# Optimization experiments

Hardware: AMD Instinct MI355X
Metric: run time of the kernel (lower is better)

The kernel has to match this reference:

```python
import jax, jax.numpy as jnp
import numpy as np


def bilinear_resize(x, out_h, out_w):
    # x: [B, C, H, W]; matches torch F.interpolate(mode='bilinear', align_corners=False)
    B, C, H, W = x.shape
    ry = jnp.clip((jnp.arange(out_h, dtype=jnp.float32) + 0.5) * (H / out_h) - 0.5, 0.0, H - 1)
    rx = jnp.clip((jnp.arange(out_w, dtype=jnp.float32) + 0.5) * (W / out_w) - 0.5, 0.0, W - 1)
    y0 = jnp.floor(ry).astype(jnp.int32); y1 = jnp.minimum(y0 + 1, H - 1)
    x0 = jnp.floor(rx).astype(jnp.int32); x1 = jnp.minimum(x0 + 1, W - 1)
    wy = (ry - y0)[:, None]  # [out_h,1]
    wx = (rx - x0)[None, :]  # [1,out_w]
    r0 = x[:, :, y0, :]; r1 = x[:, :, y1, :]
    v00 = r0[:, :, :, x0]; v01 = r0[:, :, :, x1]
    v10 = r1[:, :, :, x0]; v11 = r1[:, :, :, x1]
    return (v00 * (1 - wx) + v01 * wx) * (1 - wy) + (v10 * (1 - wx) + v11 * wx) * wy


def setup_inputs() -> dict:
    key0 = jax.random.key(0)
    ks = jax.random.split(key0, 16)
    B, N, C, H = 2, 300, 256, 8
    hw_lvl = np.array([[64, 64], [32, 32], [16, 16]], dtype=np.int64)
    L = int((hw_lvl[:, 0] * hw_lvl[:, 1]).sum())  # 5376
    p = lambda k, sh: (0.02 * jax.random.normal(k, sh, dtype=jnp.float32))
    return {
        'query': jax.random.normal(ks[0], (B, N, C), dtype=jnp.float32),
        'key': jax.random.normal(ks[1], (B, L, C), dtype=jnp.float32),
        'value': jax.random.normal(ks[2], (B, L, C), dtype=jnp.float32),
        'key_padding_mask': jnp.zeros((B, L), dtype=bool),
        'hw_lvl': hw_lvl,
        'Wq': p(ks[3], (C, C)), 'Wk': p(ks[4], (C, C)), 'Wv': p(ks[5], (C, C)),
        'Wp': p(ks[6], (C, C)), 'bp': jnp.zeros((C,), jnp.float32),
        'W1': p(ks[7], (H, H)), 'b1': jnp.zeros((H,), jnp.float32),
        'W2': p(ks[8], (H, H)), 'b2': jnp.zeros((H,), jnp.float32),
        'W3': p(ks[9], (H, H)), 'b3': jnp.zeros((H,), jnp.float32),
        'Wm': p(ks[10], (3 * H, 1)), 'bm': jnp.zeros((1,), jnp.float32),
    }


def reference(query, key, value, key_padding_mask, hw_lvl,
              Wq, Wk, Wv, Wp, bp, W1, b1, W2, b2, W3, b3, Wm, bm):
    hw = np.asarray(hw_lvl)
    h1, wd1 = int(hw[0, 0]), int(hw[0, 1])
    h2, wd2 = int(hw[1, 0]), int(hw[1, 1])
    h3, wd3 = int(hw[2, 0]), int(hw[2, 1])
    w1 = h1 * wd1
    w2 = w1 + h2 * wd2
    B, N, C = query.shape
    L = key.shape[1]
    H = W1.shape[0]
    scale = (C // H) ** -0.5

    q = (query @ Wq).reshape(B, N, H, C // H)
    k = (key @ Wk).reshape(B, L, H, C // H)
    v = (value @ Wv).reshape(B, L, H, C // H)
    attn = jnp.einsum('bnhd,blhd->bhnl', q, k) * scale  # [B,H,N,L]

    ap = attn.transpose(0, 2, 3, 1)  # [B,N,L,H]
    f1 = jax.nn.relu(ap[:, :, :w1] @ W1 + b1)                      # [B,N,w1,H]
    f2 = jax.nn.relu(ap[:, :, w1:w2] @ W2 + b2)                    # [B,N,h2*wd2,H]
    f3 = jax.nn.relu(ap[:, :, w2:] @ W3 + b3)                      # [B,N,h3*wd3,H]
    f2 = f2.transpose(0, 1, 3, 2).reshape(B * N, H, h2, wd2)
    f3 = f3.transpose(0, 1, 3, 2).reshape(B * N, H, h3, wd3)
    f2 = bilinear_resize(f2, h1, wd1).transpose(0, 2, 3, 1).reshape(B, N, w1, H)
    f3 = bilinear_resize(f3, h1, wd1).transpose(0, 2, 3, 1).reshape(B, N, w1, H)
    new_feats = jnp.concatenate([f1, f2, f3], axis=-1)             # [B,N,w1,3H]
    mask = jax.nn.relu(new_feats @ Wm + bm)                        # [B,N,w1,1]

    aw = jax.nn.softmax(attn, axis=-1)                             # [B,H,N,L]
    x = jnp.einsum('bhnl,blhd->bnhd', aw, v).reshape(B, N, C)
    x = x @ Wp + bp
    return x, mask
```

## Files before the change

kernel.cpp:

```cpp
#include <hip/hip_runtime.h>
#include <hip/hip_bf16.h>

typedef __hip_bfloat16 bf16;
typedef __attribute__((ext_vector_type(8))) short short8v;
typedef __attribute__((ext_vector_type(8))) unsigned short ushort8v;
typedef __attribute__((ext_vector_type(4))) unsigned short ushort4v;
typedef __attribute__((ext_vector_type(4))) float float4v;

__device__ __forceinline__ float bfu2f(unsigned short u) {
    union { unsigned int i; float f; } v; v.i = ((unsigned int)u) << 16; return v.f;
}
__device__ __forceinline__ unsigned short f2bfu_rn(float x) {
    union { float f; unsigned int i; } u; u.f = x;
    unsigned int r = (u.i + 0x7FFFu + ((u.i >> 16) & 1u)) >> 16;
    return (unsigned short)r;
}

__global__ __launch_bounds__(256) void cast_wt(
    const float* __restrict__ Wq, const float* __restrict__ Wk,
    const float* __restrict__ Wv, const float* __restrict__ Wp,
    unsigned short* __restrict__ wt)
{
    __shared__ unsigned short tile[64][72];
    const float* W = (blockIdx.z == 0) ? Wq : (blockIdx.z == 1) ? Wk
                   : (blockIdx.z == 2) ? Wv : Wp;
    unsigned short* WT = wt + (size_t)blockIdx.z * 65536;
    const int t = threadIdx.x;
    const int k0 = blockIdx.x * 64, n0 = blockIdx.y * 64;
    {
        const int r = t >> 2, cseg = (t & 3) * 16;
        const float* src = W + (size_t)(k0 + r) * 256 + n0 + cseg;
        #pragma unroll
        for (int j = 0; j < 16; ++j) tile[r][cseg + j] = f2bfu_rn(src[j]);
    }
    __syncthreads();
    {
        const int ch = t & 63, lq = t >> 6;
        ushort8v o0, o1;
        #pragma unroll
        for (int i = 0; i < 8; ++i) o0[i] = tile[lq * 16 + i][ch];
        #pragma unroll
        for (int i = 0; i < 8; ++i) o1[i] = tile[lq * 16 + 8 + i][ch];
        unsigned short* dst = WT + (size_t)(n0 + ch) * 256 + k0 + lq * 16;
        *(ushort8v*)(dst)     = o0;
        *(ushort8v*)(dst + 8) = o1;
    }
}

__device__ __forceinline__ void proj_core(
    const float* __restrict__ aptr, const unsigned short* __restrict__ Wt,
    int nc0, int m16, int quad, float4v acc[8])
{
    #pragma unroll
    for (int i = 0; i < 8; ++i) acc[i] = (float4v){0.f, 0.f, 0.f, 0.f};
    #pragma unroll
    for (int ks = 0; ks < 8; ++ks) {
        float4 a0 = *(const float4*)(aptr + ks * 32);
        float4 a1 = *(const float4*)(aptr + ks * 32 + 4);
        short8v af;
        af[0] = (short)f2bfu_rn(a0.x); af[1] = (short)f2bfu_rn(a0.y);
        af[2] = (short)f2bfu_rn(a0.z); af[3] = (short)f2bfu_rn(a0.w);
        af[4] = (short)f2bfu_rn(a1.x); af[5] = (short)f2bfu_rn(a1.y);
        af[6] = (short)f2bfu_rn(a1.z); af[7] = (short)f2bfu_rn(a1.w);
        #pragma unroll
        for (int i = 0; i < 8; ++i) {
            short8v bfr = *(const short8v*)(Wt + (size_t)(nc0 + i * 16 + m16) * 256 + ks * 32 + quad * 8);
            acc[i] = __builtin_amdgcn_mfma_f32_16x16x32_bf16(af, bfr, acc[i], 0, 0, 0);
        }
    }
}

__global__ __launch_bounds__(256) void proj_all(
    const float* __restrict__ q, const float* __restrict__ k, const float* __restrict__ v,
    const unsigned short* __restrict__ wt,
    unsigned short* __restrict__ qb, unsigned short* __restrict__ kb,
    unsigned short* __restrict__ vt)
{
    const int t = threadIdx.x;
    const int wave = t >> 6, lane = t & 63;
    const int m16 = lane & 15, quad = lane >> 4;
    const int msub = (wave & 1) * 16;
    const int nc0 = (wave >> 1) * 128;
    const int bx = blockIdx.x;

    float4v acc[8];
    if (bx < 19) {
        const int m0 = bx * 32;
        const int arow = min(m0 + msub + m16, 599);
        proj_core(q + (size_t)arow * 256 + quad * 8, wt, nc0, m16, quad, acc);
        #pragma unroll
        for (int i = 0; i < 8; ++i)
            #pragma unroll
            for (int r = 0; r < 4; ++r) {
                int m = m0 + msub + quad * 4 + r;
                if (m < 600)
                    qb[(size_t)m * 256 + nc0 + i * 16 + m16] = f2bfu_rn(acc[i][r]);
            }
    } else if (bx < 355) {
        const int m0 = (bx - 19) * 32;
        proj_core(k + (size_t)(m0 + msub + m16) * 256 + quad * 8, wt + 65536, nc0, m16, quad, acc);
        const int bb = (m0 >= 5376) ? 1 : 0;
        const int lb0 = m0 - bb * 5376 + msub + quad * 4;
        const int hbase = (wave >> 1) * 4;
        #pragma unroll
        for (int i = 0; i < 8; ++i) {
            const int hh = hbase + (i >> 1);
            const int c16 = (i & 1) * 16;
            unsigned short* kdst = kb + ((size_t)(bb * 8 + hh) * 5376 + lb0) * 32 + c16 + m16;
            #pragma unroll
            for (int r = 0; r < 4; ++r)
                kdst[(size_t)r * 32] = f2bfu_rn(acc[i][r]);
        }
    } else {
        const int m0 = (bx - 355) * 32;
        proj_core(v + (size_t)(m0 + msub + m16) * 256 + quad * 8, wt + 131072, nc0, m16, quad, acc);
        const int bb = (m0 >= 5376) ? 1 : 0;
        const int lb0 = m0 - bb * 5376 + msub + quad * 4;
        const int g0 = lb0 >> 3, e0 = lb0 & 7;
        const int hbase = (wave >> 1) * 4;
        #pragma unroll
        for (int i = 0; i < 8; ++i) {
            const int hh = hbase + (i >> 1);
            const int cc = (i & 1) * 16 + m16;
            ushort4v p;
            #pragma unroll
            for (int r = 0; r < 4; ++r) p[r] = f2bfu_rn(acc[i][r]);
            *(ushort4v*)(vt + (((size_t)(bb * 8 + hh) * 672 + g0) * 32 + cc) * 8 + e0) = p;
        }
    }
}

__global__ __launch_bounds__(512) void attn_fused(
    const unsigned short* __restrict__ qb, const unsigned short* __restrict__ kb,
    const unsigned short* __restrict__ vt,
    const float* __restrict__ W1, const float* __restrict__ b1,
    const float* __restrict__ W2, const float* __restrict__ b2,
    const float* __restrict__ W3, const float* __restrict__ b3,
    const float* __restrict__ Wm,
    float* __restrict__ xbp, float* __restrict__ Sp,
    float* __restrict__ g2, float* __restrict__ g3, float* __restrict__ maskp)
{
    __shared__ unsigned short probs[8][16 * 136];
    __shared__ float wT[64];
    __shared__ float blv[8], wmv[8];

    const int t = threadIdx.x;
    const int wave = t >> 6, lane = t & 63;

    const int i0 = blockIdx.x;
    const int m = (i0 & 7) * 200 + (i0 >> 3);
    if (m >= 1596) return;
    const int grp = m / 19, nt = m - grp * 19;
    const int b = grp / 42, zz = grp - b * 42;
    const int n0 = nt * 16;
    const int l0 = zz * 128;
    const int lvl = (zz >= 32) + (zz >= 40);

    const float* Wl = (lvl == 0) ? W1 : (lvl == 1) ? W2 : W3;
    const float* bl = (lvl == 0) ? b1 : (lvl == 1) ? b2 : b3;
    if (t < 64) wT[t] = Wl[(t & 7) * 8 + (t >> 3)];
    if (t < 8)  { blv[t] = bl[t]; wmv[t] = Wm[lvl * 8 + t]; }

    const int m16 = lane & 15, quad = lane >> 4;
    const int h = wave;
    const float scale = 0.17677669529663687f;

    const unsigned short* kbase = kb + ((size_t)(b * 8 + h) * 5376 + l0) * 32 + quad * 8;
    const unsigned short* vtb = vt + ((size_t)(b * 8 + h) * 672 + (l0 >> 3)) * 256 + quad * 256 + m16 * 8;
    unsigned short* const pw = &probs[wave][0];

    short8v vb[8];
    #pragma unroll
    for (int s = 0; s < 4; ++s) {
        vb[2 * s]     = *(const short8v*)(vtb + s * 1024);
        vb[2 * s + 1] = *(const short8v*)(vtb + s * 1024 + 128);
    }
    const short8v qfrag = *(const short8v*)(qb + (size_t)(b * 300 + min(n0 + m16, 299)) * 256 + h * 32 + quad * 8);

    #pragma unroll
    for (int i = 0; i < 8; ++i) {
        short8v kf = *(const short8v*)(kbase + (size_t)(i * 16 + m16) * 32);
        float4v c = {0.f, 0.f, 0.f, 0.f};
        c = __builtin_amdgcn_mfma_f32_16x16x32_bf16(kf, qfrag, c, 0, 0, 0);
        ushort4v pk;
        #pragma unroll
        for (int r = 0; r < 4; ++r) pk[r] = f2bfu_rn(c[r] * scale);
        *(ushort4v*)(pw + m16 * 136 + i * 16 + quad * 4) = pk;
    }

    float4v c0 = {0.f, 0.f, 0.f, 0.f};
    float4v c1 = {0.f, 0.f, 0.f, 0.f};
    float sm0 = 0.f, sm1 = 0.f;
    #pragma unroll
    for (int step = 0; step < 4; ++step) {
        const int lloc = step * 32 + quad * 8;
        ushort8v ua = *(const ushort8v*)(pw + m16 * 136 + lloc);
        short8v af;
        #pragma unroll
        for (int j = 0; j < 8; ++j) {
            float e = __expf(bfu2f(ua[j]));
            if (j & 1) sm1 += e; else sm0 += e;
            af[j] = (short)f2bfu_rn(e);
        }
        c0 = __builtin_amdgcn_mfma_f32_16x16x32_bf16(af, vb[2 * step],     c0, 0, 0, 0);
        c1 = __builtin_amdgcn_mfma_f32_16x16x32_bf16(af, vb[2 * step + 1], c1, 0, 0, 0);
    }

    __syncthreads();

    {
        const int nl = t >> 5;
        const int n = n0 + nl;
        if (n < 300) {
            const int lb = (t & 31) * 4;
            ushort4v u[8];
            #pragma unroll
            for (int hp = 0; hp < 8; ++hp)
                u[hp] = *(const ushort4v*)(&probs[hp][nl * 136 + lb]);
            float4 o;
            float* op = (float*)&o;
            #pragma unroll
            for (int half = 0; half < 2; ++half) {
                float sv[2][8];
                #pragma unroll
                for (int pp = 0; pp < 2; ++pp)
                    #pragma unroll
                    for (int hp = 0; hp < 8; ++hp) sv[pp][hp] = bfu2f(u[hp][half * 2 + pp]);
                float f0 = 0.f, f1 = 0.f;
                #pragma unroll
                for (int hh = 0; hh < 8; ++hh) {
                    const float4 wA = *(const float4*)(&wT[hh * 8]);
                    const float4 wB = *(const float4*)(&wT[hh * 8 + 4]);
                    const float bb_ = blv[hh], wm_ = wmv[hh];
                    float a0 = bb_
                        + sv[0][0] * wA.x + sv[0][1] * wA.y + sv[0][2] * wA.z + sv[0][3] * wA.w
                        + sv[0][4] * wB.x + sv[0][5] * wB.y + sv[0][6] * wB.z + sv[0][7] * wB.w;
                    float a1 = bb_
                        + sv[1][0] * wA.x + sv[1][1] * wA.y + sv[1][2] * wA.z + sv[1][3] * wA.w
                        + sv[1][4] * wB.x + sv[1][5] * wB.y + sv[1][6] * wB.z + sv[1][7] * wB.w;
                    f0 += fmaxf(a0, 0.f) * wm_;
                    f1 += fmaxf(a1, 0.f) * wm_;
                }
                op[half * 2]     = f0;
                op[half * 2 + 1] = f1;
            }
            const size_t bn = (size_t)(b * 300 + n);
            const int p = l0 + lb;
            float* dst = (lvl == 0) ? maskp + bn * 4096 + p
                       : (lvl == 1) ? g2 + bn * 1024 + (p - 4096)
                       :              g3 + bn * 256  + (p - 5120);
            *(float4*)dst = o;
        }
    }

    float sm = sm0 + sm1;
    sm += __shfl_xor(sm, 16);
    sm += __shfl_xor(sm, 32);
    float* xplane = xbp + (size_t)zz * 153600;
    float* splane = Sp + (size_t)zz * 4800;
    if (lane < 16 && n0 + lane < 300)
        splane[(size_t)(b * 300 + n0 + lane) * 8 + h] = sm;
    #pragma unroll
    for (int r = 0; r < 4; ++r) {
        const int n = n0 + quad * 4 + r;
        if (n < 300) {
            float* o = xplane + (size_t)(b * 300 + n) * 256 + h * 32 + m16;
            o[0]  = c0[r];
            o[16] = c1[r];
        }
    }
}

__global__ __launch_bounds__(256) void finish(
    const float* __restrict__ g2, const float* __restrict__ g3,
    const float* __restrict__ xbp, const float* __restrict__ Sp,
    float* __restrict__ xr, float* __restrict__ Sr,
    const float* __restrict__ bmp, float* __restrict__ out)
{
    const int t = threadIdx.x;
    if (blockIdx.x < 600) {
        __shared__ float gs[1280];
        __shared__ float bms;
        const int bn = blockIdx.x;
        if (t == 0) bms = bmp[0];
        ((float4v*)gs)[t] = ((const float4v*)(g2 + (size_t)bn * 1024))[t];
        if (t < 64) ((float4v*)(gs + 1024))[t] = ((const float4v*)(g3 + (size_t)bn * 256))[t];
        __syncthreads();

        float* mp = out + 153600 + (size_t)bn * 4096;
        #pragma unroll
        for (int it = 0; it < 4; ++it) {
            const int p0 = it * 1024 + t * 4;
            float4v mv = *(const float4v*)(mp + p0);
            float4v res;
            #pragma unroll
            for (int pp = 0; pp < 4; ++pp) {
                const int p = p0 + pp;
                const int Y = p >> 6, X = p & 63;
                float acc = mv[pp] + bms;
                {
                    float ry = fminf(fmaxf(0.5f * Y - 0.25f, 0.f), 31.f);
                    float rx = fminf(fmaxf(0.5f * X - 0.25f, 0.f), 31.f);
                    int y0 = (int)ry, x0 = (int)rx;
                    int y1 = min(y0 + 1, 31), x1 = min(x0 + 1, 31);
                    float wy = ry - (float)y0, wx = rx - (float)x0;
                    acc += (gs[y0 * 32 + x0] * (1.f - wx) + gs[y0 * 32 + x1] * wx) * (1.f - wy)
                         + (gs[y1 * 32 + x0] * (1.f - wx) + gs[y1 * 32 + x1] * wx) * wy;
                }
                {
                    float ry = fminf(fmaxf(0.25f * Y - 0.375f, 0.f), 15.f);
                    float rx = fminf(fmaxf(0.25f * X - 0.375f, 0.f), 15.f);
                    int y0 = (int)ry, x0 = (int)rx;
                    int y1 = min(y0 + 1, 15), x1 = min(x0 + 1, 15);
                    float wy = ry - (float)y0, wx = rx - (float)x0;
                    acc += (gs[1024 + y0 * 16 + x0] * (1.f - wx) + gs[1024 + y0 * 16 + x1] * wx) * (1.f - wy)
                         + (gs[1024 + y1 * 16 + x0] * (1.f - wx) + gs[1024 + y1 * 16 + x1] * wx) * wy;
                }
                res[pp] = fmaxf(acc, 0.f);
            }
            *(float4v*)(mp + p0) = res;
        }
    } else {
        const int idx = (blockIdx.x - 600) * 256 + t;
        if (idx < 38400) {
            float4v s = {0.f, 0.f, 0.f, 0.f};
            #pragma unroll 7
            for (int z = 0; z < 42; ++z)
                s += *(const float4v*)(xbp + (size_t)z * 153600 + (size_t)idx * 4);
            *(float4v*)(xr + (size_t)idx * 4) = s;
        } else if (idx < 38400 + 1200) {
            const int si = (idx - 38400) * 4;
            float4v s = {0.f, 0.f, 0.f, 0.f};
            #pragma unroll 7
            for (int z = 0; z < 42; ++z)
                s += *(const float4v*)(Sp + (size_t)z * 4800 + si);
            *(float4v*)(Sr + si) = s;
        }
    }
}

__global__ __launch_bounds__(256) void proj_out(
    const float* __restrict__ xr, const float* __restrict__ Sr,
    const unsigned short* __restrict__ Wtp,
    const float* __restrict__ bpv, float* __restrict__ out)
{
    const int t = threadIdx.x;
    const int wave = t >> 6, lane = t & 63;
    const int m16 = lane & 15, quad = lane >> 4;
    const int nc0 = wave * 64;
    const int m0 = blockIdx.x * 16;
    const int arow = min(m0 + m16, 599);
    const float* a0p = xr + (size_t)arow * 256 + quad * 8;

    float4v acc[4];
    #pragma unroll
    for (int i = 0; i < 4; ++i) acc[i] = (float4v){0.f, 0.f, 0.f, 0.f};

    #pragma unroll
    for (int ks = 0; ks < 8; ++ks) {
        const float rS = 1.0f / Sr[(size_t)arow * 8 + ks];
        float4 x0 = *(const float4*)(a0p + ks * 32);
        float4 x1 = *(const float4*)(a0p + ks * 32 + 4);
        short8v af;
        af[0] = (short)f2bfu_rn(x0.x * rS); af[1] = (short)f2bfu_rn(x0.y * rS);
        af[2] = (short)f2bfu_rn(x0.z * rS); af[3] = (short)f2bfu_rn(x0.w * rS);
        af[4] = (short)f2bfu_rn(x1.x * rS); af[5] = (short)f2bfu_rn(x1.y * rS);
        af[6] = (short)f2bfu_rn(x1.z * rS); af[7] = (short)f2bfu_rn(x1.w * rS);
        #pragma unroll
        for (int i = 0; i < 4; ++i) {
            short8v bfr = *(const short8v*)(Wtp + (size_t)(nc0 + i * 16 + m16) * 256 + ks * 32 + quad * 8);
            acc[i] = __builtin_amdgcn_mfma_f32_16x16x32_bf16(af, bfr, acc[i], 0, 0, 0);
        }
    }

    #pragma unroll
    for (int i = 0; i < 4; ++i) {
        const float bv = bpv[nc0 + i * 16 + m16];
        #pragma unroll
        for (int r = 0; r < 4; ++r) {
            int mm = m0 + quad * 4 + r;
            if (mm < 600)
                out[(size_t)mm * 256 + nc0 + i * 16 + m16] = acc[i][r] + bv;
        }
    }
}

extern "C" void kernel_launch(void* const* d_in, const int* in_sizes, int n_in,
                              void* d_out, int out_size, void* d_ws, size_t ws_size,
                              hipStream_t stream) {
    const float* query = (const float*)d_in[0];
    const float* key   = (const float*)d_in[1];
    const float* value = (const float*)d_in[2];
    const float* Wq = (const float*)d_in[5];
    const float* Wk = (const float*)d_in[6];
    const float* Wv = (const float*)d_in[7];
    const float* Wp = (const float*)d_in[8];
    const float* bp = (const float*)d_in[9];
    const float* W1 = (const float*)d_in[10];
    const float* b1 = (const float*)d_in[11];
    const float* W2 = (const float*)d_in[12];
    const float* b2 = (const float*)d_in[13];
    const float* W3 = (const float*)d_in[14];
    const float* b3 = (const float*)d_in[15];
    const float* Wm = (const float*)d_in[16];
    const float* bm = (const float*)d_in[17];
    float* out = (float*)d_out;

    char* ws = (char*)d_ws;
    unsigned short* wt = (unsigned short*)(ws);
    bf16*  qb   = (bf16*) (ws + 524288);
    bf16*  kb   = (bf16*) (ws + 831488);
    bf16*  vt   = (bf16*) (ws + 6336512);
    float* xbp  = (float*)(ws + 11841536);
    float* Sp   = (float*)(ws + 37646336);
    float* g2   = (float*)(ws + 38452736);
    float* g3   = (float*)(ws + 40910336);
    float* xr   = (float*)(ws + 41524736);
    float* Sr   = (float*)(ws + 42139136);
    float* maskp = out + 153600;

    cast_wt<<<dim3(4, 4, 4), 256, 0, stream>>>(Wq, Wk, Wv, Wp, wt);

    proj_all<<<691, 256, 0, stream>>>(query, key, value, wt,
        (unsigned short*)qb, (unsigned short*)kb, (unsigned short*)vt);

    attn_fused<<<1600, 512, 0, stream>>>(
        (const unsigned short*)qb, (const unsigned short*)kb, (const unsigned short*)vt,
        W1, b1, W2, b2, W3, b3, Wm, xbp, Sp, g2, g3, maskp);

    finish<<<755, 256, 0, stream>>>(g2, g3, xbp, Sp, xr, Sr, bm, out);

    proj_out<<<38, 256, 0, stream>>>(xr, Sr, (const unsigned short*)wt + 196608, bp, out);
}
```

Before: 189.1 us.

## Fuse split-K reduction with output projection and store partials before mask stage

The separate proj_out kernel is merged into finish: each of 38 extra blocks reduces the 42 split-K partial planes for its 16 rows straight into shared memory, then runs the bf16 MFMA projection in the same block. This removes one kernel launch and the xr/Sr round trip through global memory. The per-head partial x and softmax-sum stores in attn_fused now happen before the barrier and mask epilogue, so they can overlap with the mask work. In exchange, the reduction now runs on only 38 blocks instead of about 155, which may lower memory parallelism for the roughly 26MB partial read.

```diff
diff --git a/kernel.cpp b/kernel.cpp
--- a/kernel.cpp
+++ b/kernel.cpp
@@ -204,6 +204,23 @@
         }
         c0 = __builtin_amdgcn_mfma_f32_16x16x32_bf16(af, vb[2 * step],     c0, 0, 0, 0);
         c1 = __builtin_amdgcn_mfma_f32_16x16x32_bf16(af, vb[2 * step + 1], c1, 0, 0, 0);
+    }
+
+    float sm = sm0 + sm1;
+    sm += __shfl_xor(sm, 16);
+    sm += __shfl_xor(sm, 32);
+    float* xplane = xbp + (size_t)zz * 153600;
+    float* splane = Sp + (size_t)zz * 4800;
+    if (lane < 16 && n0 + lane < 300)
+        splane[(size_t)(b * 300 + n0 + lane) * 8 + h] = sm;
+    #pragma unroll
+    for (int r = 0; r < 4; ++r) {
+        const int n = n0 + quad * 4 + r;
+        if (n < 300) {
+            float* o = xplane + (size_t)(b * 300 + n) * 256 + h * 32 + m16;
+            o[0]  = c0[r];
+            o[16] = c1[r];
+        }
     }
 
     __syncthreads();
@@ -252,30 +269,14 @@
             *(float4*)dst = o;
         }
     }
-
-    float sm = sm0 + sm1;
-    sm += __shfl_xor(sm, 16);
-    sm += __shfl_xor(sm, 32);
-    float* xplane = xbp + (size_t)zz * 153600;
-    float* splane = Sp + (size_t)zz * 4800;
-    if (lane < 16 && n0 + lane < 300)
-        splane[(size_t)(b * 300 + n0 + lane) * 8 + h] = sm;
-    #pragma unroll
-    for (int r = 0; r < 4; ++r) {
-        const int n = n0 + quad * 4 + r;
-        if (n < 300) {
-            float* o = xplane + (size_t)(b * 300 + n) * 256 + h * 32 + m16;
-            o[0]  = c0[r];
-            o[16] = c1[r];
-        }
-    }
 }
 
 __global__ __launch_bounds__(256) void finish(
     const float* __restrict__ g2, const float* __restrict__ g3,
     const float* __restrict__ xbp, const float* __restrict__ Sp,
-    float* __restrict__ xr, float* __restrict__ Sr,
-    const float* __restrict__ bmp, float* __restrict__ out)
+    const unsigned short* __restrict__ Wtp,
+    const float* __restrict__ bpv, const float* __restrict__ bmp,
+    float* __restrict__ out)
 {
     const int t = threadIdx.x;
     if (blockIdx.x < 600) {
@@ -321,66 +322,77 @@
             *(float4v*)(mp + p0) = res;
         }
     } else {
-        const int idx = (blockIdx.x - 600) * 256 + t;
-        if (idx < 38400) {
-            float4v s = {0.f, 0.f, 0.f, 0.f};
-            #pragma unroll 7
+        __shared__ float xs[16][260];
+        __shared__ float Ss[16][8];
+        const int bx = blockIdx.x - 600;
+        const int m0 = bx * 16;
+
+        {
+            const int r = t >> 4, seg = t & 15;
+            const int arow = min(m0 + r, 599);
+            const float* src = xbp + (size_t)arow * 256 + seg * 16;
+            float4v s0 = {0.f,0.f,0.f,0.f}, s1 = {0.f,0.f,0.f,0.f};
+            float4v s2 = {0.f,0.f,0.f,0.f}, s3 = {0.f,0.f,0.f,0.f};
+            #pragma unroll 6
+            for (int z = 0; z < 42; ++z) {
+                const float* p = src + (size_t)z * 153600;
+                s0 += *(const float4v*)(p);
+                s1 += *(const float4v*)(p + 4);
+                s2 += *(const float4v*)(p + 8);
+                s3 += *(const float4v*)(p + 12);
+            }
+            float* d = &xs[r][seg * 16];
+            *(float4v*)(d)      = s0;
+            *(float4v*)(d + 4)  = s1;
+            *(float4v*)(d + 8)  = s2;
+            *(float4v*)(d + 12) = s3;
+        }
+        if (t < 128) {
+            const int r = t >> 3, ks = t & 7;
+            const int arow = min(m0 + r, 599);
+            float s = 0.f;
+            #pragma unroll 6
             for (int z = 0; z < 42; ++z)
-                s += *(const float4v*)(xbp + (size_t)z * 153600 + (size_t)idx * 4);
-            *(float4v*)(xr + (size_t)idx * 4) = s;
-        } else if (idx < 38400 + 1200) {
-            const int si = (idx - 38400) * 4;
-            float4v s = {0.f, 0.f, 0.f, 0.f};
-            #pragma unroll 7
-            for (int z = 0; z < 42; ++z)
-                s += *(const float4v*)(Sp + (size_t)z * 4800 + si);
-            *(float4v*)(Sr + si) = s;
-        }
-    }
-}
-
-__global__ __launch_bounds__(256) void proj_out(
-    const float* __restrict__ xr, const float* __restrict__ Sr,
-    const unsigned short* __restrict__ Wtp,
-    const float* __restrict__ bpv, float* __restrict__ out)
-{
-    const int t = threadIdx.x;
-    const int wave = t >> 6, lane = t & 63;
-    const int m16 = lane & 15, quad = lane >> 4;
-    const int nc0 = wave * 64;
-    const int m0 = blockIdx.x * 16;
-    const int arow = min(m0 + m16, 599);
-    const float* a0p = xr + (size_t)arow * 256 + quad * 8;
-
-    float4v acc[4];
-    #pragma unroll
-    for (int i = 0; i < 4; ++i) acc[i] = (float4v){0.f, 0.f, 0.f, 0.f};
-
-    #pragma unroll
-    for (int ks = 0; ks < 8; ++ks) {
-        const float rS = 1.0f / Sr[(size_t)arow * 8 + ks];
-        float4 x0 = *(const float4*)(a0p + ks * 32);
-        float4 x1 = *(const float4*)(a0p + ks * 32 + 4);
-        short8v af;
-        af[0] = (short)f2bfu_rn(x0.x * rS); af[1] = (short)f2bfu_rn(x0.y * rS);
-        af[2] = (short)f2bfu_rn(x0.z * rS); af[3] = (short)f2bfu_rn(x0.w * rS);
-        af[4] = (short)f2bfu_rn(x1.x * rS); af[5] = (short)f2bfu_rn(x1.y * rS);
-        af[6] = (short)f2bfu_rn(x1.z * rS); af[7] = (short)f2bfu_rn(x1.w * rS);
+                s += Sp[(size_t)z * 4800 + (size_t)arow * 8 + ks];
+            Ss[r][ks] = s;
+        }
+        __syncthreads();
+
+        const int wave = t >> 6, lane = t & 63;
+        const int m16 = lane & 15, quad = lane >> 4;
+        const int nc0 = wave * 64;
+
+        float4v acc[4];
+        #pragma unroll
+        for (int i = 0; i < 4; ++i) acc[i] = (float4v){0.f, 0.f, 0.f, 0.f};
+
+        #pragma unroll
+        for (int ks = 0; ks < 8; ++ks) {
+            const float rS = 1.0f / Ss[m16][ks];
+            const float* xp = &xs[m16][ks * 32 + quad * 8];
+            float4 x0 = *(const float4*)(xp);
+            float4 x1 = *(const float4*)(xp + 4);
+            short8v af;
+            af[0] = (short)f2bfu_rn(x0.x * rS); af[1] = (short)f2bfu_rn(x0.y * rS);
+            af[2] = (short)f2bfu_rn(x0.z * rS); af[3] = (short)f2bfu_rn(x0.w * rS);
+            af[4] = (short)f2bfu_rn(x1.x * rS); af[5] = (short)f2bfu_rn(x1.y * rS);
+            af[6] = (short)f2bfu_rn(x1.z * rS); af[7] = (short)f2bfu_rn(x1.w * rS);
+            #pragma unroll
+            for (int i = 0; i < 4; ++i) {
+                short8v bfr = *(const short8v*)(Wtp + (size_t)(nc0 + i * 16 + m16) * 256 + ks * 32 + quad * 8);
+                acc[i] = __builtin_amdgcn_mfma_f32_16x16x32_bf16(af, bfr, acc[i], 0, 0, 0);
+            }
+        }
+
         #pragma unroll
         for (int i = 0; i < 4; ++i) {
-            short8v bfr = *(const short8v*)(Wtp + (size_t)(nc0 + i * 16 + m16) * 256 + ks * 32 + quad * 8);
-            acc[i] = __builtin_amdgcn_mfma_f32_16x16x32_bf16(af, bfr, acc[i], 0, 0, 0);
-        }
-    }
-
-    #pragma unroll
-    for (int i = 0; i < 4; ++i) {
-        const float bv = bpv[nc0 + i * 16 + m16];
-        #pragma unroll
-        for (int r = 0; r < 4; ++r) {
-            int mm = m0 + quad * 4 + r;
-            if (mm < 600)
-                out[(size_t)mm * 256 + nc0 + i * 16 + m16] = acc[i][r] + bv;
+            const float bv = bpv[nc0 + i * 16 + m16];
+            #pragma unroll
+            for (int r = 0; r < 4; ++r) {
+                int mm = m0 + quad * 4 + r;
+                if (mm < 600)
+                    out[(size_t)mm * 256 + nc0 + i * 16 + m16] = acc[i][r] + bv;
+            }
         }
     }
 }
@@ -415,8 +427,6 @@
     float* Sp   = (float*)(ws + 37646336);
     float* g2   = (float*)(ws + 38452736);
     float* g3   = (float*)(ws + 40910336);
-    float* xr   = (float*)(ws + 41524736);
-    float* Sr   = (float*)(ws + 42139136);
     float* maskp = out + 153600;
 
     cast_wt<<<dim3(4, 4, 4), 256, 0, stream>>>(Wq, Wk, Wv, Wp, wt);
@@ -428,7 +438,6 @@
         (const unsigned short*)qb, (const unsigned short*)kb, (const unsigned short*)vt,
         W1, b1, W2, b2, W3, b3, Wm, xbp, Sp, g2, g3, maskp);
 
-    finish<<<755, 256, 0, stream>>>(g2, g3, xbp, Sp, xr, Sr, bm, out);
-
-    proj_out<<<38, 256, 0, stream>>>(xr, Sr, (const unsigned short*)wt + 196608, bp, out);
-}
+    finish<<<638, 256, 0, stream>>>(g2, g3, xbp, Sp,
+        (const unsigned short*)wt + 196608, bp, bm, out);
+}
```

Measured after the change: 182.6 us. 3.4% less time.
